# Optimization experiments

Hardware: AMD Instinct MI355X
Metric: run time of the kernel (lower is better)

Reference implementation:

```python
import jax, jax.numpy as jnp
import numpy as np

N, IN_C, HID, OUT_C = 4096, 512, 512, 40
E = 131072
N_CLUSTERS, PCA_K, KMEANS_ITERS = 7, 10, 10
EPS = 1e-12


def _linear_params(key, fin, fout):
    k1, k2 = jax.random.split(key)
    lim = 1.0 / np.sqrt(fin)
    W = jax.random.uniform(k1, (fin, fout), jnp.float32, -lim, lim)
    b = jax.random.uniform(k2, (fout,), jnp.float32, -lim, lim)
    return W, b


def setup_inputs() -> dict:
    key = jax.random.key(0)
    ks = jax.random.split(key, 8)
    x = jax.random.normal(ks[0], (N, IN_C), jnp.float32)
    edge_index = jax.random.randint(ks[1], (2, E), 0, N, dtype=jnp.int32)
    y = jax.random.randint(ks[2], (N,), 0, N_CLUSTERS, dtype=jnp.int32)
    W_ego, b_ego = _linear_params(ks[3], IN_C, HID)
    W_cos, b_cos = _linear_params(ks[4], IN_C, HID)
    W_glob, b_glob = _linear_params(ks[5], IN_C, HID)
    W_fc, b_fc = _linear_params(ks[6], HID + IN_C + HID + HID, OUT_C)
    return dict(x=x, W_ego=W_ego, b_ego=b_ego, W_cos=W_cos, b_cos=b_cos,
                W_glob=W_glob, b_glob=b_glob, W_fc=W_fc, b_fc=b_fc,
                edge_index=edge_index, y=y)


def _mp_layer(x, W, b, src, dst):
    # MessagePassingLayer: scatter-add lin(x)[src] at dst, then relu
    h = x @ W + b
    agg = jax.ops.segment_sum(h[src], dst, num_segments=N)
    return jax.nn.relu(agg)


def _dominant_mask(x):
    # Dominant branch: PCA(10) -> KMeans(n_clusters) -> keep nodes with dist <= median.
    # sklearn's randomized KMeans replaced by deterministic Lloyd iterations
    # (init = first N_CLUSTERS rows); whole pipeline is detached in the original.
    xs = jax.lax.stop_gradient(x)
    xc = xs - xs.mean(0, keepdims=True)
    _, _, vt = jnp.linalg.svd(xc, full_matrices=False)
    feats = xc @ vt[:PCA_K].T  # [N, PCA_K]

    def step(c, _):
        d2 = ((feats[:, None, :] - c[None]) ** 2).sum(-1)  # [N, K]
        lab = jnp.argmin(d2, axis=1)
        sums = jax.ops.segment_sum(feats, lab, num_segments=N_CLUSTERS)
        cnt = jax.ops.segment_sum(jnp.ones((N,), jnp.float32), lab, num_segments=N_CLUSTERS)
        newc = jnp.where(cnt[:, None] > 0, sums / jnp.maximum(cnt, 1.0)[:, None], c)
        return newc, None

    centers, _ = jax.lax.scan(step, feats[:N_CLUSTERS], None, length=KMEANS_ITERS)
    d2 = ((feats[:, None, :] - centers[None]) ** 2).sum(-1)
    lab = jnp.argmin(d2, axis=1)
    dist = jnp.linalg.norm(feats - centers[lab], axis=1)
    keep = dist <= jnp.median(dist)
    return jax.lax.stop_gradient(keep.astype(jnp.float32))


def _forward(x, W_ego, b_ego, W_cos, b_cos, W_glob, b_glob, W_fc, b_fc, src, dst):
    # --- ego branch: exact 2-hop (source_to_target) subgraph mean per node ---
    # B[i, j] = 1 iff edge j->i; subset(i) = {i} | 1-hop | 2-hop (set semantics via >0)
    B = jnp.zeros((N, N), jnp.float32).at[dst, src].add(1.0)
    reach = jnp.eye(N, dtype=jnp.float32) + B + B @ B
    Mf = (reach > 0).astype(jnp.float32)
    ego_feats = (Mf @ x) / Mf.sum(1, keepdims=True)

    # --- Dominant branch: zero out far-from-center nodes ---
    keep = _dominant_mask(x)
    cut_enc = x * keep[:, None]

    # --- cosine branch: segment softmax over outgoing edges grouped by src ---
    norm_x = x / jnp.maximum(jnp.linalg.norm(x, axis=1, keepdims=True), EPS)
    sims = (norm_x[src] * norm_x[dst]).sum(-1)  # [E]
    smax = jax.ops.segment_max(sims, src, num_segments=N)
    ex = jnp.exp(sims - smax[src])
    den = jax.ops.segment_sum(ex, src, num_segments=N)
    w = ex / jnp.maximum(den, EPS)[src]
    num = jax.ops.segment_sum(w[:, None] * x[dst], src, num_segments=N)
    wsum = jax.ops.segment_sum(w, src, num_segments=N)
    deg = jax.ops.segment_sum(jnp.ones((E,), jnp.float32), src, num_segments=N)
    cos_feats = jnp.where(deg[:, None] > 0, num / jnp.maximum(wsum, EPS)[:, None], x)

    # --- encoders + head ---
    global_feats = x @ W_glob + b_glob
    ego_enc = _mp_layer(ego_feats, W_ego, b_ego, src, dst)
    cosine_enc = _mp_layer(cos_feats, W_cos, b_cos, src, dst)
    combined = jnp.concatenate([ego_enc, cut_enc, cosine_enc, global_feats], axis=-1)
    return jax.nn.log_softmax(combined @ W_fc + b_fc, axis=1)


def reference(x, W_ego, b_ego, W_cos, b_cos, W_glob, b_glob, W_fc, b_fc, edge_index, y):
    src, dst = edge_index[0], edge_index[1]
    return _forward(x, W_ego, b_ego, W_cos, b_cos, W_glob, b_glob, W_fc, b_fc, src, dst)
```

## Files before the change

### kernel.cpp

```cpp
#include <hip/hip_runtime.h>
#include <hip/hip_cooperative_groups.h>
#include <math.h>

namespace cg = cooperative_groups;

#define NN 4096
#define NC 512
#define NE 131072

typedef __bf16 bf16x8 __attribute__((ext_vector_type(8)));
typedef float f32x4 __attribute__((ext_vector_type(4)));
typedef unsigned short u16x8 __attribute__((ext_vector_type(8)));

__device__ __forceinline__ unsigned short f2b(float f){
  unsigned u = __float_as_uint(f);
  u += 0x7fffu + ((u >> 16) & 1u);
  return (unsigned short)(u >> 16);
}
__device__ __forceinline__ float b2f(unsigned short h){
  return __uint_as_float(((unsigned)h) << 16);
}
__device__ __forceinline__ float wredsum(float v){
  #pragma unroll
  for (int o = 32; o; o >>= 1) v += __shfl_xor(v, o, 64);
  return v;
}
__device__ __forceinline__ float wredmax(float v){
  #pragma unroll
  for (int o = 32; o; o >>= 1) v = fmaxf(v, __shfl_xor(v, o, 64));
  return v;
}

__global__ __launch_bounds__(256) void k_zero(unsigned long long* __restrict__ B1,
    int* __restrict__ cnt_in, int* __restrict__ cnt_out, double* __restrict__ meanbuf){
  int id = blockIdx.x*256 + threadIdx.x;
  B1[id] = 0ull;
  if (id < NN){ cnt_in[id] = 0; cnt_out[id] = 0; }
  if (id < 512) meanbuf[id] = 0.0;
}

__global__ __launch_bounds__(256) void k_transconv(const float* __restrict__ src, int R, int C,
    unsigned short* __restrict__ dstT, int ldT, unsigned short* __restrict__ dstD){
  __shared__ unsigned short tile[64][65];
  int bc = blockIdx.x * 64, br = blockIdx.y * 64;
  int t = threadIdx.x, lc = t & 63, lr4 = t >> 6;
  for (int j = 0; j < 16; ++j){
    int r = br + lr4*16 + j, c = bc + lc;
    float v = (r < R && c < C) ? src[(size_t)r*C + c] : 0.f;
    unsigned short b = f2b(v);
    tile[lr4*16+j][lc] = b;
    if (dstD && r < R && c < C) dstD[(size_t)r*C + c] = b;
  }
  __syncthreads();
  for (int j = 0; j < 16; ++j){
    int cc = bc + lr4*16 + j, rr = br + lc;
    if (cc < C && rr < R) dstT[(size_t)cc*ldT + rr] = tile[lc][lr4*16+j];
  }
}

__global__ __launch_bounds__(256) void k_transconv3(const float* __restrict__ A,
    const float* __restrict__ B, const float* __restrict__ C,
    unsigned short* __restrict__ TA, unsigned short* __restrict__ TB, unsigned short* __restrict__ TC){
  __shared__ unsigned short tile[64][65];
  const float* src = (blockIdx.z == 0) ? A : ((blockIdx.z == 1) ? B : C);
  unsigned short* dstT = (blockIdx.z == 0) ? TA : ((blockIdx.z == 1) ? TB : TC);
  int bc = blockIdx.x * 64, br = blockIdx.y * 64;
  int t = threadIdx.x, lc = t & 63, lr4 = t >> 6;
  for (int j = 0; j < 16; ++j){
    int r = br + lr4*16 + j, c = bc + lc;
    tile[lr4*16+j][lc] = f2b(src[(size_t)r*512 + c]);
  }
  __syncthreads();
  for (int j = 0; j < 16; ++j){
    int cc = bc + lr4*16 + j, rr = br + lc;
    dstT[(size_t)cc*512 + rr] = tile[lc][lr4*16+j];
  }
}

__global__ __launch_bounds__(256) void k_normx(const float* __restrict__ x, unsigned short* __restrict__ nx){
  int wid = threadIdx.x >> 6, lane = threadIdx.x & 63;
  int row = blockIdx.x*4 + wid;
  const float* xr = x + (size_t)row*NC + lane*8;
  float v[8]; float ss = 0.f;
  #pragma unroll
  for (int j=0;j<8;j++){ v[j] = xr[j]; ss += v[j]*v[j]; }
  ss = wredsum(ss);
  float sc = 1.0f / fmaxf(sqrtf(ss), 1e-12f);
  u16x8 o;
  #pragma unroll
  for (int j=0;j<8;j++) o[j] = f2b(v[j]*sc);
  *(u16x8*)(nx + (size_t)row*NC + lane*8) = o;
}

__global__ void k_count_b1(const int* __restrict__ src, const int* __restrict__ dst,
    int* cin, int* cout, unsigned long long* B1){
  int e = blockIdx.x*256 + threadIdx.x;
  if (e < NE){
    int s = src[e], d = dst[e];
    atomicAdd(&cout[s], 1);
    atomicAdd(&cin[d], 1);
    atomicOr(&B1[(size_t)d*64 + (s>>6)], 1ull << (s & 63));
  }
}
__global__ __launch_bounds__(1024) void k_scan(const int* __restrict__ cnt0, const int* __restrict__ cnt1,
    int* off0, int* off1, int* fill0, int* fill1){
  __shared__ int s[1024];
  int t = threadIdx.x;
  for (int arr = 0; arr < 2; ++arr){
    const int* cnt = arr ? cnt1 : cnt0;
    int* off = arr ? off1 : off0;
    int* fill = arr ? fill1 : fill0;
    int a0 = cnt[t*4], a1 = cnt[t*4+1], a2 = cnt[t*4+2], a3 = cnt[t*4+3];
    int ts = a0+a1+a2+a3;
    s[t] = ts; __syncthreads();
    for (int o = 1; o < 1024; o <<= 1){
      int v = (t >= o) ? s[t-o] : 0; __syncthreads();
      s[t] += v; __syncthreads();
    }
    int ex = s[t] - ts;
    off[t*4] = ex; off[t*4+1] = ex+a0; off[t*4+2] = ex+a0+a1; off[t*4+3] = ex+a0+a1+a2;
    fill[t*4] = ex; fill[t*4+1] = ex+a0; fill[t*4+2] = ex+a0+a1; fill[t*4+3] = ex+a0+a1+a2;
    if (t == 1023) off[4096] = s[1023];
    __syncthreads();
  }
}
__global__ void k_fill(const int* __restrict__ src, const int* __restrict__ dst,
    int* fin, int* fout, int* csr_in, int* csr_out){
  int e = blockIdx.x*256 + threadIdx.x;
  if (e < NE){
    int s = src[e], d = dst[e];
    int pi = atomicAdd(&fin[d], 1);  csr_in[pi] = s;
    int po = atomicAdd(&fout[s], 1); csr_out[po] = d;
  }
}

__global__ __launch_bounds__(256) void k_bits2(const unsigned long long* __restrict__ B1,
    const int* __restrict__ off_in, const int* __restrict__ csr_in,
    unsigned short* __restrict__ Mf, float* __restrict__ rowrecip){
  int wid = threadIdx.x >> 6, lane = threadIdx.x & 63;
  int node = blockIdx.x*4 + wid;
  unsigned long long bits = B1[(size_t)node*64 + lane];
  if (lane == (node >> 6)) bits |= 1ull << (node & 63);
  int beg = off_in[node], end = off_in[node+1];
  for (int e = beg; e < end; ++e){
    int j = csr_in[e];
    bits |= B1[(size_t)j*64 + lane];
  }
  int pc = __popcll(bits);
  #pragma unroll
  for (int o = 32; o; o >>= 1) pc += __shfl_xor(pc, o, 64);
  if (lane == 0) rowrecip[node] = 1.0f / (float)pc;
  unsigned lo = (unsigned)(bits & 0xffffffffull), hi = (unsigned)(bits >> 32);
  unsigned int* Mrow = (unsigned int*)(Mf + (size_t)node*NN);
  for (int k = 0; k < 32; ++k){
    int srcl = 2*k + (lane >> 5);
    unsigned wlo = (unsigned)__shfl((int)lo, srcl, 64);
    unsigned whi = (unsigned)__shfl((int)hi, srcl, 64);
    unsigned long long w2 = ((unsigned long long)whi << 32) | wlo;
    int sh = (lane & 31) * 2;
    unsigned v = (unsigned)((w2 >> sh) & 3ull);
    Mrow[k*64 + lane] = ((v & 1u) ? 0x3F80u : 0u) | ((v & 2u) ? 0x3F800000u : 0u);
  }
}

template<int MODE>
__global__ __launch_bounds__(256) void gemm_bt(
    const unsigned short* __restrict__ A, int lda,
    const unsigned short* __restrict__ BT, int ldb,
    int K, int nstore,
    float* __restrict__ outF, unsigned short* __restrict__ outB, int ldc,
    const float* __restrict__ bias, const float* __restrict__ rowscale){
  __shared__ unsigned short Asm[64*40];
  __shared__ unsigned short Bsm[128*40];
  const int t = threadIdx.x;
  const int lane = t & 63, wid = t >> 6;
  const int wm = wid >> 1, wn = wid & 1;
  const int row0 = blockIdx.x * 64, col0 = blockIdx.y * 128;
  f32x4 acc[2][4];
  #pragma unroll
  for (int a = 0; a < 2; a++)
    #pragma unroll
    for (int b = 0; b < 4; b++){ acc[a][b][0]=0.f; acc[a][b][1]=0.f; acc[a][b][2]=0.f; acc[a][b][3]=0.f; }

  const int ar = t >> 2, as = t & 3;
  const unsigned short* Ap  = A  + (size_t)(row0 + ar)*lda + as*8;
  const unsigned short* Bp0 = BT + (size_t)(col0 + ar)*ldb + as*8;
  const unsigned short* Bp1 = BT + (size_t)(col0 + ar + 64)*ldb + as*8;
  unsigned short* Asd  = &Asm[ar*40 + as*8];
  unsigned short* Bsd0 = &Bsm[ar*40 + as*8];
  unsigned short* Bsd1 = &Bsm[(ar+64)*40 + as*8];

  const int fr = lane & 15, q = lane >> 4;
  const int aoff = (wm*32 + fr)*40 + q*8;
  const int boff = (wn*64 + fr)*40 + q*8;

  for (int k0 = 0; k0 < K; k0 += 32){
    *(u16x8*)Asd  = *(const u16x8*)(Ap  + k0);
    *(u16x8*)Bsd0 = *(const u16x8*)(Bp0 + k0);
    *(u16x8*)Bsd1 = *(const u16x8*)(Bp1 + k0);
    __syncthreads();
    bf16x8 af0 = *(const bf16x8*)&Asm[aoff];
    bf16x8 af1 = *(const bf16x8*)&Asm[aoff + 16*40];
    bf16x8 bfr[4];
    #pragma unroll
    for (int b = 0; b < 4; b++) bfr[b] = *(const bf16x8*)&Bsm[boff + b*16*40];
    #pragma unroll
    for (int b = 0; b < 4; b++){
      acc[0][b] = __builtin_amdgcn_mfma_f32_16x16x32_bf16(af0, bfr[b], acc[0][b], 0, 0, 0);
      acc[1][b] = __builtin_amdgcn_mfma_f32_16x16x32_bf16(af1, bfr[b], acc[1][b], 0, 0, 0);
    }
    __syncthreads();
  }
  #pragma unroll
  for (int a = 0; a < 2; a++){
    const int grow0 = row0 + wm*32 + a*16 + q*4;
    #pragma unroll
    for (int b = 0; b < 4; b++){
      const int gcol = col0 + wn*64 + b*16 + fr;
      if (gcol < nstore){
        #pragma unroll
        for (int r = 0; r < 4; r++){
          const int grow = grow0 + r;
          float v = acc[a][b][r];
          if (MODE == 0){ v *= rowscale[grow]; outB[(size_t)grow*ldc + gcol] = f2b(v); }
          if (MODE == 1){ v += bias[gcol];     outB[(size_t)grow*ldc + gcol] = f2b(v); }
          if (MODE == 2){ v += bias[gcol];     outF[(size_t)grow*ldc + gcol] = v; }
        }
      }
    }
  }
}

__global__ __launch_bounds__(256) void gemm_bt3(
    const unsigned short* __restrict__ A0, const unsigned short* __restrict__ A1, const unsigned short* __restrict__ A2,
    const unsigned short* __restrict__ B0, const unsigned short* __restrict__ B1g, const unsigned short* __restrict__ B2,
    const float* __restrict__ bias0, const float* __restrict__ bias1, const float* __restrict__ bias2,
    unsigned short* __restrict__ o0, unsigned short* __restrict__ o1, unsigned short* __restrict__ o2,
    int ldc2){
  const int z = blockIdx.z;
  const unsigned short* A  = (z == 0) ? A0 : ((z == 1) ? A1 : A2);
  const unsigned short* BT = (z == 0) ? B0 : ((z == 1) ? B1g : B2);
  const float* bias        = (z == 0) ? bias0 : ((z == 1) ? bias1 : bias2);
  unsigned short* outB     = (z == 0) ? o0 : ((z == 1) ? o1 : o2);
  const int ldc = (z == 2) ? ldc2 : 512;

  __shared__ unsigned short Asm[64*40];
  __shared__ unsigned short Bsm[128*40];
  const int t = threadIdx.x;
  const int lane = t & 63, wid = t >> 6;
  const int wm = wid >> 1, wn = wid & 1;
  const int row0 = blockIdx.x * 64, col0 = blockIdx.y * 128;
  f32x4 acc[2][4];
  #pragma unroll
  for (int a = 0; a < 2; a++)
    #pragma unroll
    for (int b = 0; b < 4; b++){ acc[a][b][0]=0.f; acc[a][b][1]=0.f; acc[a][b][2]=0.f; acc[a][b][3]=0.f; }

  const int ar = t >> 2, as = t & 3;
  const unsigned short* Ap  = A  + (size_t)(row0 + ar)*512 + as*8;
  const unsigned short* Bp0 = BT + (size_t)(col0 + ar)*512 + as*8;
  const unsigned short* Bp1 = BT + (size_t)(col0 + ar + 64)*512 + as*8;
  unsigned short* Asd  = &Asm[ar*40 + as*8];
  unsigned short* Bsd0 = &Bsm[ar*40 + as*8];
  unsigned short* Bsd1 = &Bsm[(ar+64)*40 + as*8];

  const int fr = lane & 15, q = lane >> 4;
  const int aoff = (wm*32 + fr)*40 + q*8;
  const int boff = (wn*64 + fr)*40 + q*8;

  for (int k0 = 0; k0 < 512; k0 += 32){
    *(u16x8*)Asd  = *(const u16x8*)(Ap  + k0);
    *(u16x8*)Bsd0 = *(const u16x8*)(Bp0 + k0);
    *(u16x8*)Bsd1 = *(const u16x8*)(Bp1 + k0);
    __syncthreads();
    bf16x8 af0 = *(const bf16x8*)&Asm[aoff];
    bf16x8 af1 = *(const bf16x8*)&Asm[aoff + 16*40];
    bf16x8 bfr[4];
    #pragma unroll
    for (int b = 0; b < 4; b++) bfr[b] = *(const bf16x8*)&Bsm[boff + b*16*40];
    #pragma unroll
    for (int b = 0; b < 4; b++){
      acc[0][b] = __builtin_amdgcn_mfma_f32_16x16x32_bf16(af0, bfr[b], acc[0][b], 0, 0, 0);
      acc[1][b] = __builtin_amdgcn_mfma_f32_16x16x32_bf16(af1, bfr[b], acc[1][b], 0, 0, 0);
    }
    __syncthreads();
  }
  #pragma unroll
  for (int a = 0; a < 2; a++){
    const int grow0 = row0 + wm*32 + a*16 + q*4;
    #pragma unroll
    for (int b = 0; b < 4; b++){
      const int gcol = col0 + wn*64 + b*16 + fr;
      #pragma unroll
      for (int r = 0; r < 4; r++){
        const int grow = grow0 + r;
        float v = acc[a][b][r] + bias[gcol];
        outB[(size_t)grow*ldc + gcol] = f2b(v);
      }
    }
  }
}

__global__ __launch_bounds__(256) void gemm_head(
    const unsigned short* __restrict__ A, const unsigned short* __restrict__ BT,
    const float* __restrict__ bias, float* __restrict__ out){
  __shared__ unsigned short Asm[64*40];
  __shared__ unsigned short Bsm[128*40];
  __shared__ float lg[64][41];
  const int t = threadIdx.x;
  const int lane = t & 63, wid = t >> 6;
  const int wm = wid >> 1, wn = wid & 1;
  const int row0 = blockIdx.x * 64;
  f32x4 acc[2][4];
  #pragma unroll
  for (int a = 0; a < 2; a++)
    #pragma unroll
    for (int b = 0; b < 4; b++){ acc[a][b][0]=0.f; acc[a][b][1]=0.f; acc[a][b][2]=0.f; acc[a][b][3]=0.f; }

  const int ar = t >> 2, as = t & 3;
  const unsigned short* Ap  = A  + (size_t)(row0 + ar)*2048 + as*8;
  const unsigned short* Bp0 = BT + (size_t)ar*2048 + as*8;
  const unsigned short* Bp1 = BT + (size_t)(ar + 64)*2048 + as*8;
  unsigned short* Asd  = &Asm[ar*40 + as*8];
  unsigned short* Bsd0 = &Bsm[ar*40 + as*8];
  unsigned short* Bsd1 = &Bsm[(ar+64)*40 + as*8];

  const int fr = lane & 15, q = lane >> 4;
  const int aoff = (wm*32 + fr)*40 + q*8;
  const int boff = (wn*64 + fr)*40 + q*8;

  for (int k0 = 0; k0 < 2048; k0 += 32){
    *(u16x8*)Asd  = *(const u16x8*)(Ap  + k0);
    *(u16x8*)Bsd0 = *(const u16x8*)(Bp0 + k0);
    *(u16x8*)Bsd1 = *(const u16x8*)(Bp1 + k0);
    __syncthreads();
    bf16x8 af0 = *(const bf16x8*)&Asm[aoff];
    bf16x8 af1 = *(const bf16x8*)&Asm[aoff + 16*40];
    bf16x8 bfr[4];
    #pragma unroll
    for (int b = 0; b < 4; b++) bfr[b] = *(const bf16x8*)&Bsm[boff + b*16*40];
    #pragma unroll
    for (int b = 0; b < 4; b++){
      acc[0][b] = __builtin_amdgcn_mfma_f32_16x16x32_bf16(af0, bfr[b], acc[0][b], 0, 0, 0);
      acc[1][b] = __builtin_amdgcn_mfma_f32_16x16x32_bf16(af1, bfr[b], acc[1][b], 0, 0, 0);
    }
    __syncthreads();
  }
  if (wn == 0){
    #pragma unroll
    for (int a = 0; a < 2; a++){
      const int lrow0 = wm*32 + a*16 + q*4;
      #pragma unroll
      for (int b = 0; b < 4; b++){
        const int gcol = b*16 + fr;
        if (gcol < 40){
          #pragma unroll
          for (int r = 0; r < 4; r++)
            lg[lrow0 + r][gcol] = acc[a][b][r] + bias[gcol];
        }
      }
    }
  }
  __syncthreads();
  if (t < 64){
    float m = -3.0e38f;
    #pragma unroll
    for (int j = 0; j < 40; ++j) m = fmaxf(m, lg[t][j]);
    float s = 0.f;
    #pragma unroll
    for (int j = 0; j < 40; ++j) s += expf(lg[t][j] - m);
    float l = logf(s);
    float* orow = out + (size_t)(row0 + t)*40;
    #pragma unroll
    for (int j = 0; j < 40; ++j) orow[j] = lg[t][j] - m - l;
  }
}

__global__ __launch_bounds__(256) void k_cos(const unsigned short* __restrict__ nx,
    const unsigned short* __restrict__ xb,
    const int* __restrict__ off_out, const int* __restrict__ csr_out,
    unsigned short* __restrict__ cosf){
  __shared__ float simsb[4][256];
  int wid = threadIdx.x >> 6, lane = threadIdx.x & 63;
  int node = blockIdx.x*4 + wid;
  float own[8];
  { u16x8 o = *(const u16x8*)(nx + (size_t)node*NC + lane*8);
    #pragma unroll
    for (int j=0;j<8;j++) own[j] = b2f(o[j]); }
  int beg = off_out[node], end = off_out[node+1], deg = end - beg;
  float m = -3.0e38f;
  for (int e = 0; e < deg; ++e){
    int d = csr_out[beg+e];
    u16x8 nb = *(const u16x8*)(nx + (size_t)d*NC + lane*8);
    float sp = 0.f;
    #pragma unroll
    for (int j=0;j<8;j++) sp += own[j]*b2f(nb[j]);
    float s = wredsum(sp);
    if (e < 256 && lane == 0) simsb[wid][e] = s;
    m = fmaxf(m, s);
  }
  float den = 0.f, acc[8] = {0,0,0,0,0,0,0,0};
  for (int e = 0; e < deg; ++e){
    int d = csr_out[beg+e];
    float s;
    if (e < 256) s = simsb[wid][e];
    else {
      u16x8 nb = *(const u16x8*)(nx + (size_t)d*NC + lane*8);
      float sp = 0.f;
      #pragma unroll
      for (int j=0;j<8;j++) sp += own[j]*b2f(nb[j]);
      s = wredsum(sp);
    }
    float w = expf(s - m);
    den += w;
    u16x8 xv = *(const u16x8*)(xb + (size_t)d*NC + lane*8);
    #pragma unroll
    for (int j=0;j<8;j++) acc[j] += w * b2f(xv[j]);
  }
  u16x8 o;
  if (deg > 0){
    float r = 1.0f/den;
    #pragma unroll
    for (int j=0;j<8;j++) o[j] = f2b(acc[j]*r);
  } else {
    o = *(const u16x8*)(xb + (size_t)node*NC + lane*8);
  }
  *(u16x8*)(cosf + (size_t)node*NC + lane*8) = o;
}

__global__ __launch_bounds__(256) void k_aggcut(const unsigned short* __restrict__ he,
    const unsigned short* __restrict__ hc,
    const int* __restrict__ off_in, const int* __restrict__ csr_in,
    const unsigned short* __restrict__ xb, const float* __restrict__ keep,
    unsigned short* __restrict__ comb){
  int wid = threadIdx.x >> 6, lane = threadIdx.x & 63;
  int node = blockIdx.x*4 + wid;
  float ae[8] = {0,0,0,0,0,0,0,0}, ac[8] = {0,0,0,0,0,0,0,0};
  int beg = off_in[node], end = off_in[node+1];
  for (int e = beg; e < end; ++e){
    int j = csr_in[e];
    u16x8 ve = *(const u16x8*)(he + (size_t)j*NC + lane*8);
    u16x8 vc = *(const u16x8*)(hc + (size_t)j*NC + lane*8);
    #pragma unroll
    for (int k=0;k<8;k++){ ae[k] += b2f(ve[k]); ac[k] += b2f(vc[k]); }
  }
  u16x8 oe, oc;
  #pragma unroll
  for (int k=0;k<8;k++){ oe[k] = f2b(fmaxf(ae[k], 0.f)); oc[k] = f2b(fmaxf(ac[k], 0.f)); }
  *(u16x8*)(comb + (size_t)node*2048 + lane*8) = oe;
  *(u16x8*)(comb + (size_t)node*2048 + 1024 + lane*8) = oc;
  u16x8 xv = *(const u16x8*)(xb + (size_t)node*NC + lane*8);
  if (keep[node] == 0.f){
    #pragma unroll
    for (int j=0;j<8;j++) xv[j] = 0;
  }
  *(u16x8*)(comb + (size_t)node*2048 + 512 + lane*8) = xv;
}

__global__ void k_colmean(const float* __restrict__ x, double* __restrict__ meanbuf){
  int c0 = threadIdx.x;
  int r0 = blockIdx.x*128;
  double s0 = 0, s1 = 0;
  for (int r = r0; r < r0+128; ++r){
    s0 += (double)x[(size_t)r*NC + c0];
    s1 += (double)x[(size_t)r*NC + c0 + 256];
  }
  atomicAdd(&meanbuf[c0], s0);
  atomicAdd(&meanbuf[c0+256], s1);
}

__global__ __launch_bounds__(256) void k_cov(const float* __restrict__ x,
    const double* __restrict__ meanbuf, double* __restrict__ Cm){
  const int bi = blockIdx.x, bj = blockIdx.y;
  if (bi > bj) return;
  __shared__ float sa[16][33];
  __shared__ float sb[16][33];
  const int t = threadIdx.x;
  const int ti = t & 15, tj = t >> 4;
  int l0 = t, l1 = t + 256;
  int r0a = l0 >> 5, c0a = l0 & 31;
  int r1a = l1 >> 5, c1a = l1 & 31;
  float ma0 = (float)(meanbuf[bi*32 + c0a] * (1.0/4096.0));
  float ma1 = (float)(meanbuf[bi*32 + c1a] * (1.0/4096.0));
  float mb0 = (float)(meanbuf[bj*32 + c0a] * (1.0/4096.0));
  float mb1 = (float)(meanbuf[bj*32 + c1a] * (1.0/4096.0));
  double a00=0,a01=0,a10=0,a11=0;
  for (int r0 = 0; r0 < NN; r0 += 16){
    sa[r0a][c0a] = x[(size_t)(r0 + r0a)*NC + bi*32 + c0a] - ma0;
    sa[r1a][c1a] = x[(size_t)(r0 + r1a)*NC + bi*32 + c1a] - ma1;
    sb[r0a][c0a] = x[(size_t)(r0 + r0a)*NC + bj*32 + c0a] - mb0;
    sb[r1a][c1a] = x[(size_t)(r0 + r1a)*NC + bj*32 + c1a] - mb1;
    __syncthreads();
    #pragma unroll
    for (int rr = 0; rr < 16; ++rr){
      double av0 = (double)sa[rr][ti], av1 = (double)sa[rr][ti+16];
      double bv0 = (double)sb[rr][tj], bv1 = (double)sb[rr][tj+16];
      a00 += av0*bv0; a01 += av0*bv1; a10 += av1*bv0; a11 += av1*bv1;
    }
    __syncthreads();
  }
  const int r0i = bi*32+ti, r1i = bi*32+ti+16, c0j = bj*32+tj, c1j = bj*32+tj+16;
  Cm[(size_t)r0i*512 + c0j] = a00;
  Cm[(size_t)r0i*512 + c1j] = a01;
  Cm[(size_t)r1i*512 + c0j] = a10;
  Cm[(size_t)r1i*512 + c1j] = a11;
  if (bi < bj){
    Cm[(size_t)c0j*512 + r0i] = a00;
    Cm[(size_t)c1j*512 + r0i] = a01;
    Cm[(size_t)c0j*512 + r1i] = a10;
    Cm[(size_t)c1j*512 + r1i] = a11;
  }
}

__global__ __launch_bounds__(256) void k_mm64(const double* __restrict__ A,
    const double* __restrict__ B, double* __restrict__ C){
  const int bi = blockIdx.x, bj = blockIdx.y;
  if (bi > bj) return;
  __shared__ double sa[32][17];
  __shared__ double sb[16][33];
  const int t = threadIdx.x;
  const int ti = t & 15, tj = t >> 4;
  double a00=0,a01=0,a10=0,a11=0;
  for (int k0 = 0; k0 < 512; k0 += 16){
    { int ii = t >> 4, kk = t & 15;
      sa[ii][kk] = A[(size_t)(bi*32+ii)*512 + k0+kk];
      int ii2 = (t+256) >> 4, kk2 = (t+256) & 15;
      sa[ii2][kk2] = A[(size_t)(bi*32+ii2)*512 + k0+kk2];
      int kk3 = t >> 5, jj3 = t & 31;
      sb[kk3][jj3] = B[(size_t)(k0+kk3)*512 + bj*32+jj3];
      int kk4 = (t+256) >> 5, jj4 = (t+256) & 31;
      sb[kk4][jj4] = B[(size_t)(k0+kk4)*512 + bj*32+jj4];
    }
    __syncthreads();
    #pragma unroll
    for (int kk = 0; kk < 16; ++kk){
      double av0 = sa[ti][kk], av1 = sa[ti+16][kk];
      double bv0 = sb[kk][tj], bv1 = sb[kk][tj+16];
      a00 += av0*bv0; a01 += av0*bv1; a10 += av1*bv0; a11 += av1*bv1;
    }
    __syncthreads();
  }
  const int r0i = bi*32+ti, r1i = bi*32+ti+16, c0j = bj*32+tj, c1j = bj*32+tj+16;
  C[(size_t)r0i*512 + c0j] = a00;
  C[(size_t)r0i*512 + c1j] = a01;
  C[(size_t)r1i*512 + c0j] = a10;
  C[(size_t)r1i*512 + c1j] = a11;
  if (bi < bj){
    C[(size_t)c0j*512 + r0i] = a00;
    C[(size_t)c1j*512 + r0i] = a01;
    C[(size_t)c0j*512 + r1i] = a10;
    C[(size_t)c1j*512 + r1i] = a11;
  }
}

union TailSmem {
  double red[256];
  double L[32][33];
  struct {
    double G[32][33], H[32][33], Q[32][33];
    double pcs[16], pss[16];
    int pp[16], pq[16], map[32], idx[10];
    double eig[32];
  } jac;
  struct {
    float cs[7][10];
    float fs[256][10];
    unsigned char labs[256];
    float sums[77];
  } km;
  struct {
    unsigned u[4096];
    int redc[4];
  } med;
};

__device__ __forceinline__ void matv_step(const double* __restrict__ M,
    const double* __restrict__ Vin, double* __restrict__ Vout, double scale, int gid){
  int r = gid >> 5, c = gid & 31;
  const double* Mr = M + (size_t)r*512;
  double s0=0,s1=0,s2=0,s3=0;
  for (int k = 0; k < 512; k += 4){
    s0 += Mr[k]   * Vin[(size_t)k*32 + c];
    s1 += Mr[k+1] * Vin[(size_t)(k+1)*32 + c];
    s2 += Mr[k+2] * Vin[(size_t)(k+2)*32 + c];
    s3 += Mr[k+3] * Vin[(size_t)(k+3)*32 + c];
  }
  Vout[gid] = ((s0+s1)+(s2+s3))*scale;
}

__global__ __launch_bounds__(256) void k_tail(
    const double* __restrict__ Cm, const double* __restrict__ C16m, const double* __restrict__ C64m,
    double* __restrict__ Va, double* __restrict__ Vb, double* __restrict__ Yb, double* __restrict__ Gm,
    const float* __restrict__ x, const double* __restrict__ meanbuf, float* __restrict__ Pm,
    float* __restrict__ feats, float* __restrict__ part2, float* __restrict__ distb,
    float* __restrict__ keep){
  cg::grid_group grid = cg::this_grid();
  __shared__ TailSmem sm;
  __shared__ double s_scal0, s_scal1;
  const int t = threadIdx.x;
  const int b = blockIdx.x;
  const int gid = b*256 + t;

  {
    double m0 = -1e300, m1 = -1e300;
    for (int i = t; i < 512; i += 256){
      m0 = fmax(m0, C16m[(size_t)i*512 + i]);
      m1 = fmax(m1, C64m[(size_t)i*512 + i]);
    }
    sm.red[t] = m0; __syncthreads();
    for (int o = 128; o; o >>= 1){ if (t < o) sm.red[t] = fmax(sm.red[t], sm.red[t+o]); __syncthreads(); }
    if (t == 0) s_scal0 = 1.0 / fmax(sm.red[0], 1e-300);
    __syncthreads();
    sm.red[t] = m1; __syncthreads();
    for (int o = 128; o; o >>= 1){ if (t < o) sm.red[t] = fmax(sm.red[t], sm.red[t+o]); __syncthreads(); }
    if (t == 0) s_scal1 = 1.0 / fmax(sm.red[0], 1e-300);
    __syncthreads();
  }

  {
    unsigned h = (unsigned)gid * 2654435761u + 12345u;
    h ^= h >> 13; h *= 2246822519u; h ^= h >> 16;
    Va[gid] = ((double)(h & 0xffffu) / 32768.0) - 1.0;
  }
  grid.sync();

  for (int it = 0; it < 2; ++it){
    matv_step(C64m, Va, Vb, s_scal1, gid);
    grid.sync();
    matv_step(C16m, Vb, Va, s_scal0, gid);
    grid.sync();
    if (t < 16){
      int e = b*16 + t; int i = e >> 5, j = e & 31;
      double s = 0;
      for (int k = 0; k < 512; ++k) s += Va[(size_t)k*32+i]*Va[(size_t)k*32+j];
      Gm[e] = s;
    }
    grid.sync();
    {
      for (int l = t; l < 1024; l += 256){ int i = l >> 5, j = l & 31; sm.L[i][j] = Gm[l]; }
      __syncthreads();
      for (int k = 0; k < 32; ++k){
        if (t == 0) sm.L[k][k] = sqrt(fmax(sm.L[k][k], 1e-300));
        __syncthreads();
        if (t > k && t < 32) sm.L[t][k] /= sm.L[k][k];
        __syncthreads();
        for (int l = t; l < 1024; l += 256){
          int i = l >> 5, j = l & 31;
          if (i > k && j > k && j <= i) sm.L[i][j] -= sm.L[i][k]*sm.L[j][k];
        }
        __syncthreads();
      }
      if (t < 8){
        int r = b*8 + t;
        double v[32];
        #pragma unroll
        for (int jj = 0; jj < 32; ++jj) v[jj] = Va[(size_t)r*32 + jj];
        #pragma unroll
        for (int jj = 0; jj < 32; ++jj){
          double s = v[jj];
          #pragma unroll
          for (int ii = 0; ii < 32; ++ii) if (ii < jj) s -= sm.L[jj][ii]*v[ii];
          v[jj] = s / sm.L[jj][jj];
        }
        #pragma unroll
        for (int jj = 0; jj < 32; ++jj) Va[(size_t)r*32 + jj] = v[jj];
      }
      __syncthreads();
    }
    grid.sync();
  }

  matv_step(Cm, Va, Yb, 1.0, gid);
  grid.sync();

  if (t < 16){
    int e = b*16 + t; int i = e >> 5, j = e & 31;
    double s = 0;
    for (int k = 0; k < 512; ++k) s += Va[(size_t)k*32+i]*Yb[(size_t)k*32+j];
    Gm[e] = s;
  }
  grid.sync();

  if (b == 0){
    for (int l = t; l < 1024; l += 256){
      int i = l >> 5, j = l & 31;
      sm.jac.G[i][j] = 0.5*(Gm[i*32+j] + Gm[j*32+i]);
      sm.jac.Q[i][j] = (i == j) ? 1.0 : 0.0;
    }
    __syncthreads();
    for (int sweep = 0; sweep < 5; ++sweep)
    for (int r = 0; r < 31; ++r){
      if (t < 16){
        int u = (t == 0) ? 0 : ((r + t - 1) % 31) + 1;
        int v = ((r + 30 - t) % 31) + 1;
        int p_ = u < v ? u : v, q_ = u < v ? v : u;
        double app = sm.jac.G[p_][p_], aqq = sm.jac.G[q_][q_], apq = sm.jac.G[p_][q_];
        double c, s;
        if (fabs(apq) < 1e-280){ c = 1.0; s = 0.0; }
        else {
          double tau = (aqq - app)/(2.0*apq);
          double tt = (tau >= 0 ? 1.0 : -1.0)/(fabs(tau) + sqrt(1.0 + tau*tau));
          c = 1.0/sqrt(1.0 + tt*tt); s = tt*c;
        }
        sm.jac.pcs[t] = c; sm.jac.pss[t] = s; sm.jac.pp[t] = p_; sm.jac.pq[t] = q_;
        sm.jac.map[p_] = t; sm.jac.map[q_] = t | 32;
      }
      __syncthreads();
      for (int l = t; l < 1024; l += 256){
        int i = l >> 5, j = l & 31;
        int mi = sm.jac.map[i], k = mi & 31;
        double c = sm.jac.pcs[k], s = sm.jac.pss[k];
        double gp = sm.jac.G[sm.jac.pp[k]][j], gq = sm.jac.G[sm.jac.pq[k]][j];
        sm.jac.H[i][j] = (mi & 32) ? (s*gp + c*gq) : (c*gp - s*gq);
      }
      __syncthreads();
      for (int l = t; l < 512; l += 256){
        int i = l >> 4, k = l & 15;
        double c = sm.jac.pcs[k], s = sm.jac.pss[k];
        int p_ = sm.jac.pp[k], q_ = sm.jac.pq[k];
        double hp = sm.jac.H[i][p_], hq = sm.jac.H[i][q_];
        sm.jac.G[i][p_] = c*hp - s*hq; sm.jac.G[i][q_] = s*hp + c*hq;
        double qp = sm.jac.Q[i][p_], qq = sm.jac.Q[i][q_];
        sm.jac.Q[i][p_] = c*qp - s*qq; sm.jac.Q[i][q_] = s*qp + c*qq;
      }
      __syncthreads();
    }
    if (t == 0){
      for (int i2 = 0; i2 < 32; ++i2) sm.jac.eig[i2] = sm.jac.G[i2][i2];
      unsigned used = 0;
      for (int k = 0; k < 10; ++k){
        int best = 0; double bv = -1e300;
        for (int i2 = 0; i2 < 32; ++i2)
          if (!((used >> i2) & 1u) && sm.jac.eig[i2] > bv){ bv = sm.jac.eig[i2]; best = i2; }
        used |= 1u << best; sm.jac.idx[k] = best;
      }
    }
    __syncthreads();
    for (int l = t; l < 5120; l += 256){
      int k = l/10, j = l%10;
      int c = sm.jac.idx[j];
      double s2 = 0;
      for (int m = 0; m < 32; ++m) s2 += Va[(size_t)k*32+m]*sm.jac.Q[m][c];
      Pm[k*10+j] = (float)s2;
    }
  }
  grid.sync();

  for (int id = gid; id < 65536; id += 16384){
    int n = id >> 4, j = id & 15;
    if (j < 10){
      float s = 0;
      for (int c2 = 0; c2 < 512; ++c2)
        s += (x[(size_t)n*512+c2] - (float)(meanbuf[c2]*(1.0/4096.0))) * Pm[c2*10+j];
      feats[n*10+j] = s;
    }
  }
  grid.sync();

  if (t < 70) sm.km.cs[t/10][t%10] = feats[t];
  if (b < 16){
    int base = b*256;
    for (int i = t; i < 2560; i += 256) sm.km.fs[i/10][i%10] = feats[base*10 + i];
  }
  __syncthreads();
  for (int iter = 0; iter < 10; ++iter){
    float* pbuf = part2 + (size_t)(iter & 1)*16*77;
    if (b < 16){
      float f[10];
      #pragma unroll
      for (int d = 0; d < 10; ++d) f[d] = sm.km.fs[t][d];
      int best = 0; float bd = 3.0e38f;
      for (int k = 0; k < 7; ++k){
        float s = 0;
        #pragma unroll
        for (int d = 0; d < 10; ++d){ float df = f[d]-sm.km.cs[k][d]; s += df*df; }
        if (s < bd){ bd = s; best = k; }
      }
      sm.km.labs[t] = (unsigned char)best;
      __syncthreads();
      if (t < 77){
        float acc = 0;
        if (t < 70){
          int k = t/10, d = t%10;
          for (int nn = 0; nn < 256; ++nn) if (sm.km.labs[nn] == k) acc += sm.km.fs[nn][d];
        } else {
          int k = t - 70;
          for (int nn = 0; nn < 256; ++nn) if (sm.km.labs[nn] == k) acc += 1.f;
        }
        pbuf[b*77 + t] = acc;
      }
    }
    grid.sync();
    if (t < 77){
      float s = 0;
      for (int bb = 0; bb < 16; ++bb) s += pbuf[bb*77 + t];
      sm.km.sums[t] = s;
    }
    __syncthreads();
    if (t < 70){
      float cnt = sm.km.sums[70 + t/10];
      if (cnt > 0.f) sm.km.cs[t/10][t%10] = sm.km.sums[t] / fmaxf(cnt, 1.f);
    }
    __syncthreads();
  }
  if (b < 16){
    float f[10];
    #pragma unroll
    for (int d = 0; d < 10; ++d) f[d] = sm.km.fs[t][d];
    float bd = 3.0e38f;
    for (int k = 0; k < 7; ++k){
      float s = 0;
      #pragma unroll
      for (int d = 0; d < 10; ++d){ float df = f[d]-sm.km.cs[k][d]; s += df*df; }
      bd = fminf(bd, s);
    }
    distb[b*256 + t] = sqrtf(bd);
  }
  grid.sync();

  if (b == 0){
    for (int i = t; i < 4096; i += 256) sm.med.u[i] = __float_as_uint(distb[i]);
    __syncthreads();
    unsigned vals[2];
    for (int ri = 0; ri < 2; ++ri){
      int r = 2047 + ri;
      unsigned prefix = 0;
      for (int bit = 31; bit >= 0; --bit){
        unsigned hm = (bit < 31) ? (0xffffffffu << (bit+1)) : 0u;
        int c = 0;
        for (int i = t; i < 4096; i += 256){
          unsigned e = sm.med.u[i];
          if ((e & hm) == prefix && !((e >> bit) & 1u)) c++;
        }
        #pragma unroll
        for (int o = 32; o; o >>= 1) c += __shfl_xor(c, o, 64);
        if ((t & 63) == 0) sm.med.redc[t >> 6] = c;
        __syncthreads();
        int tot = sm.med.redc[0] + sm.med.redc[1] + sm.med.redc[2] + sm.med.redc[3];
        if (r >= tot){ prefix |= (1u << bit); r -= tot; }
        __syncthreads();
      }
      vals[ri] = prefix;
    }
    float med = 0.5f*(__uint_as_float(vals[0]) + __uint_as_float(vals[1]));
    for (int i = t; i < 4096; i += 256) keep[i] = (distb[i] <= med) ? 1.f : 0.f;
  }
}

extern "C" void kernel_launch(void* const* d_in, const int* in_sizes, int n_in,
                              void* d_out, int out_size, void* d_ws, size_t ws_size,
                              hipStream_t stream){
  const float* x      = (const float*)d_in[0];
  const float* W_ego  = (const float*)d_in[1];
  const float* b_ego  = (const float*)d_in[2];
  const float* W_cos  = (const float*)d_in[3];
  const float* b_cos  = (const float*)d_in[4];
  const float* W_glob = (const float*)d_in[5];
  const float* b_glob = (const float*)d_in[6];
  const float* W_fc   = (const float*)d_in[7];
  const float* b_fc   = (const float*)d_in[8];
  const int*   ei     = (const int*)d_in[9];
  const int* src = ei;
  const int* dst = ei + NE;
  float* out = (float*)d_out;

  char* p = (char*)d_ws;
  auto alloc = [&](size_t n) -> char* { char* r = p; p += (n + 255) & ~(size_t)255; return r; };

  unsigned long long* B1 = (unsigned long long*)alloc((size_t)NN*64*8);
  unsigned short* Mf     = (unsigned short*)alloc((size_t)NN*NN*2);
  unsigned short* x_bf   = (unsigned short*)alloc((size_t)NN*NC*2);
  unsigned short* xT_bf  = (unsigned short*)alloc((size_t)NN*NC*2);
  unsigned short* nx_bf  = (unsigned short*)alloc((size_t)NN*NC*2);
  unsigned short* egof   = (unsigned short*)alloc((size_t)NN*NC*2);
  unsigned short* cosf   = (unsigned short*)alloc((size_t)NN*NC*2);
  unsigned short* h_ego  = (unsigned short*)alloc((size_t)NN*NC*2);
  unsigned short* h_cos  = (unsigned short*)alloc((size_t)NN*NC*2);
  unsigned short* WegoT  = (unsigned short*)alloc((size_t)512*512*2);
  unsigned short* WcosT  = (unsigned short*)alloc((size_t)512*512*2);
  unsigned short* WglobT = (unsigned short*)alloc((size_t)512*512*2);
  unsigned short* WfcT   = (unsigned short*)alloc((size_t)128*2048*2);
  unsigned short* comb   = (unsigned short*)alloc((size_t)NN*2048*2);
  float* rowrecip = (float*)alloc((size_t)NN*4);
  float* keep     = (float*)alloc((size_t)NN*4);
  int* cnt_in   = (int*)alloc((size_t)NN*4);
  int* cnt_out  = (int*)alloc((size_t)NN*4);
  int* off_in   = (int*)alloc((size_t)(NN+1)*4);
  int* off_out  = (int*)alloc((size_t)(NN+1)*4);
  int* fill_in  = (int*)alloc((size_t)NN*4);
  int* fill_out = (int*)alloc((size_t)NN*4);
  int* csr_in   = (int*)alloc((size_t)NE*4);
  int* csr_out  = (int*)alloc((size_t)NE*4);
  double* meanbuf = (double*)alloc(512*8);
  double* Cm  = (double*)alloc((size_t)512*512*8);
  double* C2m = (double*)alloc((size_t)512*512*8);
  double* C4m = (double*)alloc((size_t)512*512*8);
  double* C8m = (double*)alloc((size_t)512*512*8);
  double* C16m = (double*)alloc((size_t)512*512*8);
  double* C32m = (double*)alloc((size_t)512*512*8);
  double* C64m = (double*)alloc((size_t)512*512*8);
  double* Va  = (double*)alloc((size_t)512*32*8);
  double* Vb  = (double*)alloc((size_t)512*32*8);
  double* Yb  = (double*)alloc((size_t)512*32*8);
  double* Gm  = (double*)alloc(32*32*8);
  float* Pm    = (float*)alloc((size_t)512*10*4);
  float* feats = (float*)alloc((size_t)NN*10*4);
  float* part  = (float*)alloc((size_t)2*16*77*4);
  float* distb = (float*)alloc((size_t)NN*4);

  k_zero<<<1024, 256, 0, stream>>>(B1, cnt_in, cnt_out, meanbuf);

  k_transconv<<<dim3(8,64), 256, 0, stream>>>(x, NN, NC, xT_bf, NN, x_bf);
  k_transconv3<<<dim3(8,8,3), 256, 0, stream>>>(W_ego, W_cos, W_glob, WegoT, WcosT, WglobT);
  k_transconv<<<dim3(1,32), 256, 0, stream>>>(W_fc, 2048, 40, WfcT, 2048, (unsigned short*)0);
  k_normx<<<1024, 256, 0, stream>>>(x, nx_bf);

  k_count_b1<<<512, 256, 0, stream>>>(src, dst, cnt_in, cnt_out, B1);
  k_scan<<<1, 1024, 0, stream>>>(cnt_in, cnt_out, off_in, off_out, fill_in, fill_out);
  k_fill<<<512, 256, 0, stream>>>(src, dst, fill_in, fill_out, csr_in, csr_out);
  k_bits2<<<1024, 256, 0, stream>>>(B1, off_in, csr_in, Mf, rowrecip);

  gemm_bt<0><<<dim3(64,4), 256, 0, stream>>>(Mf, NN, xT_bf, NN, NN, NC,
      (float*)0, egof, NC, (const float*)0, rowrecip);

  k_colmean<<<32, 256, 0, stream>>>(x, meanbuf);
  k_cov<<<dim3(16,16), 256, 0, stream>>>(x, meanbuf, Cm);
  k_mm64<<<dim3(16,16), 256, 0, stream>>>(Cm,  Cm,  C2m);
  k_mm64<<<dim3(16,16), 256, 0, stream>>>(C2m, C2m, C4m);
  k_mm64<<<dim3(16,16), 256, 0, stream>>>(C4m, C4m, C8m);
  k_mm64<<<dim3(16,16), 256, 0, stream>>>(C8m, C8m, C16m);
  k_mm64<<<dim3(16,16), 256, 0, stream>>>(C16m, C16m, C32m);
  k_mm64<<<dim3(16,16), 256, 0, stream>>>(C32m, C32m, C64m);

  {
    void* args[] = { (void*)&Cm, (void*)&C16m, (void*)&C64m, (void*)&Va, (void*)&Vb,
                     (void*)&Yb, (void*)&Gm, (void*)&x, (void*)&meanbuf, (void*)&Pm,
                     (void*)&feats, (void*)&part, (void*)&distb, (void*)&keep };
    hipLaunchCooperativeKernel((void*)k_tail, dim3(64), dim3(256), args, 0, stream);
  }

  k_cos<<<1024, 256, 0, stream>>>(nx_bf, x_bf, off_out, csr_out, cosf);

  gemm_bt3<<<dim3(64,4,3), 256, 0, stream>>>(
      egof, cosf, x_bf,
      WegoT, WcosT, WglobT,
      b_ego, b_cos, b_glob,
      h_ego, h_cos, comb + 1536,
      2048);

  k_aggcut<<<1024, 256, 0, stream>>>(h_ego, h_cos, off_in, csr_in, x_bf, keep, comb);

  gemm_head<<<64, 256, 0, stream>>>(comb, WfcT, b_fc, out);
}
```

Before: 1.735 ms.

## Fuse cosine softmax into single pass and tile PCA projection in tail kernel

k_cos now drops the max-subtraction pass and computes cosine similarity from the bf16 features scaled by precomputed inverse norms. This lets each edge's neighbour row be loaded once, and the normalized-x buffer and its write are removed. Skipping the max shift is safe because cosine similarities are bounded in [-1,1]. Separately, the PCA feature projection in the cooperative tail kernel moves from a strided per-(node,component) loop to 16 blocks. Each thread computes all 10 components for one row, with the projection matrix and mean staged in shared memory. This trades some precision (bf16 x instead of bf16 normalized x) for fewer memory passes.

```diff
diff --git a/kernel.cpp b/kernel.cpp
--- a/kernel.cpp
+++ b/kernel.cpp
@@ -23,11 +23,6 @@
 __device__ __forceinline__ float wredsum(float v){
   #pragma unroll
   for (int o = 32; o; o >>= 1) v += __shfl_xor(v, o, 64);
-  return v;
-}
-__device__ __forceinline__ float wredmax(float v){
-  #pragma unroll
-  for (int o = 32; o; o >>= 1) v = fmaxf(v, __shfl_xor(v, o, 64));
   return v;
 }
 
@@ -77,19 +72,15 @@
   }
 }
 
-__global__ __launch_bounds__(256) void k_normx(const float* __restrict__ x, unsigned short* __restrict__ nx){
+__global__ __launch_bounds__(256) void k_invnorm(const float* __restrict__ x, float* __restrict__ invn){
   int wid = threadIdx.x >> 6, lane = threadIdx.x & 63;
   int row = blockIdx.x*4 + wid;
   const float* xr = x + (size_t)row*NC + lane*8;
-  float v[8]; float ss = 0.f;
+  float ss = 0.f;
   #pragma unroll
-  for (int j=0;j<8;j++){ v[j] = xr[j]; ss += v[j]*v[j]; }
+  for (int j=0;j<8;j++){ float v = xr[j]; ss += v*v; }
   ss = wredsum(ss);
-  float sc = 1.0f / fmaxf(sqrtf(ss), 1e-12f);
-  u16x8 o;
-  #pragma unroll
-  for (int j=0;j<8;j++) o[j] = f2b(v[j]*sc);
-  *(u16x8*)(nx + (size_t)row*NC + lane*8) = o;
+  if (lane == 0) invn[row] = 1.0f / fmaxf(sqrtf(ss), 1e-12f);
 }
 
 __global__ void k_count_b1(const int* __restrict__ src, const int* __restrict__ dst,
@@ -376,46 +367,33 @@
   }
 }
 
-__global__ __launch_bounds__(256) void k_cos(const unsigned short* __restrict__ nx,
-    const unsigned short* __restrict__ xb,
+__global__ __launch_bounds__(256) void k_cos(const unsigned short* __restrict__ xb,
+    const float* __restrict__ invn,
     const int* __restrict__ off_out, const int* __restrict__ csr_out,
     unsigned short* __restrict__ cosf){
-  __shared__ float simsb[4][256];
   int wid = threadIdx.x >> 6, lane = threadIdx.x & 63;
   int node = blockIdx.x*4 + wid;
   float own[8];
-  { u16x8 o = *(const u16x8*)(nx + (size_t)node*NC + lane*8);
+  { u16x8 o = *(const u16x8*)(xb + (size_t)node*NC + lane*8);
     #pragma unroll
     for (int j=0;j<8;j++) own[j] = b2f(o[j]); }
+  float inv_i = invn[node];
   int beg = off_out[node], end = off_out[node+1], deg = end - beg;
-  float m = -3.0e38f;
-  for (int e = 0; e < deg; ++e){
-    int d = csr_out[beg+e];
-    u16x8 nb = *(const u16x8*)(nx + (size_t)d*NC + lane*8);
-    float sp = 0.f;
-    #pragma unroll
-    for (int j=0;j<8;j++) sp += own[j]*b2f(nb[j]);
-    float s = wredsum(sp);
-    if (e < 256 && lane == 0) simsb[wid][e] = s;
-    m = fmaxf(m, s);
-  }
   float den = 0.f, acc[8] = {0,0,0,0,0,0,0,0};
   for (int e = 0; e < deg; ++e){
     int d = csr_out[beg+e];
-    float s;
-    if (e < 256) s = simsb[wid][e];
-    else {
-      u16x8 nb = *(const u16x8*)(nx + (size_t)d*NC + lane*8);
-      float sp = 0.f;
-      #pragma unroll
-      for (int j=0;j<8;j++) sp += own[j]*b2f(nb[j]);
-      s = wredsum(sp);
-    }
-    float w = expf(s - m);
+    u16x8 xv = *(const u16x8*)(xb + (size_t)d*NC + lane*8);
+    float xd[8];
+    #pragma unroll
+    for (int j=0;j<8;j++) xd[j] = b2f(xv[j]);
+    float sp = 0.f;
+    #pragma unroll
+    for (int j=0;j<8;j++) sp += own[j]*xd[j];
+    float s = wredsum(sp) * inv_i * invn[d];
+    float w = expf(s);
     den += w;
-    u16x8 xv = *(const u16x8*)(xb + (size_t)d*NC + lane*8);
-    #pragma unroll
-    for (int j=0;j<8;j++) acc[j] += w * b2f(xv[j]);
+    #pragma unroll
+    for (int j=0;j<8;j++) acc[j] += w * xd[j];
   }
   u16x8 o;
   if (deg > 0){
@@ -563,6 +541,10 @@
     double eig[32];
   } jac;
   struct {
+    float Ps[512][10];
+    float cm[512];
+  } ft;
+  struct {
     float cs[7][10];
     float fs[256][10];
     unsigned char labs[256];
@@ -746,14 +728,25 @@
   }
   grid.sync();
 
-  for (int id = gid; id < 65536; id += 16384){
-    int n = id >> 4, j = id & 15;
-    if (j < 10){
-      float s = 0;
-      for (int c2 = 0; c2 < 512; ++c2)
-        s += (x[(size_t)n*512+c2] - (float)(meanbuf[c2]*(1.0/4096.0))) * Pm[c2*10+j];
-      feats[n*10+j] = s;
-    }
+  if (b < 16){
+    for (int l = t; l < 5120; l += 256) sm.ft.Ps[l/10][l%10] = Pm[l];
+    for (int c = t; c < 512; c += 256) sm.ft.cm[c] = (float)(meanbuf[c]*(1.0/4096.0));
+    __syncthreads();
+    int r = b*256 + t;
+    float acc[10] = {0,0,0,0,0,0,0,0,0,0};
+    const float* xr = x + (size_t)r*512;
+    for (int c0 = 0; c0 < 512; c0 += 4){
+      float4 xv = *(const float4*)&xr[c0];
+      float xs[4] = {xv.x, xv.y, xv.z, xv.w};
+      #pragma unroll
+      for (int q = 0; q < 4; ++q){
+        float xc = xs[q] - sm.ft.cm[c0+q];
+        #pragma unroll
+        for (int j = 0; j < 10; ++j) acc[j] += xc * sm.ft.Ps[c0+q][j];
+      }
+    }
+    #pragma unroll
+    for (int j = 0; j < 10; ++j) feats[r*10+j] = acc[j];
   }
   grid.sync();
 
@@ -871,7 +864,6 @@
   unsigned short* Mf     = (unsigned short*)alloc((size_t)NN*NN*2);
   unsigned short* x_bf   = (unsigned short*)alloc((size_t)NN*NC*2);
   unsigned short* xT_bf  = (unsigned short*)alloc((size_t)NN*NC*2);
-  unsigned short* nx_bf  = (unsigned short*)alloc((size_t)NN*NC*2);
   unsigned short* egof   = (unsigned short*)alloc((size_t)NN*NC*2);
   unsigned short* cosf   = (unsigned short*)alloc((size_t)NN*NC*2);
   unsigned short* h_ego  = (unsigned short*)alloc((size_t)NN*NC*2);
@@ -883,6 +875,7 @@
   unsigned short* comb   = (unsigned short*)alloc((size_t)NN*2048*2);
   float* rowrecip = (float*)alloc((size_t)NN*4);
   float* keep     = (float*)alloc((size_t)NN*4);
+  float* invn     = (float*)alloc((size_t)NN*4);
   int* cnt_in   = (int*)alloc((size_t)NN*4);
   int* cnt_out  = (int*)alloc((size_t)NN*4);
   int* off_in   = (int*)alloc((size_t)(NN+1)*4);
@@ -913,7 +906,7 @@
   k_transconv<<<dim3(8,64), 256, 0, stream>>>(x, NN, NC, xT_bf, NN, x_bf);
   k_transconv3<<<dim3(8,8,3), 256, 0, stream>>>(W_ego, W_cos, W_glob, WegoT, WcosT, WglobT);
   k_transconv<<<dim3(1,32), 256, 0, stream>>>(W_fc, 2048, 40, WfcT, 2048, (unsigned short*)0);
-  k_normx<<<1024, 256, 0, stream>>>(x, nx_bf);
+  k_invnorm<<<1024, 256, 0, stream>>>(x, invn);
 
   k_count_b1<<<512, 256, 0, stream>>>(src, dst, cnt_in, cnt_out, B1);
   k_scan<<<1, 1024, 0, stream>>>(cnt_in, cnt_out, off_in, off_out, fill_in, fill_out);
@@ -939,7 +932,7 @@
     hipLaunchCooperativeKernel((void*)k_tail, dim3(64), dim3(256), args, 0, stream);
   }
 
-  k_cos<<<1024, 256, 0, stream>>>(nx_bf, x_bf, off_out, csr_out, cosf);
+  k_cos<<<1024, 256, 0, stream>>>(x_bf, invn, off_out, csr_out, cosf);
 
   gemm_bt3<<<dim3(64,4,3), 256, 0, stream>>>(
       egof, cosf, x_bf,
```

Result: faster. 1.666 ms (-4.0%).
